# Kernel optimization log

Hardware: AMD Instinct MI355X
Metric: run time of the kernel (lower is better)

The kernel has to match this reference:

```python
import jax, jax.numpy as jnp
import numpy as np

DIM = 768
H = 12
HD = DIM // H
SCALE = HD ** (-0.5)


def setup_inputs() -> dict:
    key = jax.random.key(0)
    ks = jax.random.split(key, 10)
    s = DIM ** (-0.5)
    x = jax.random.normal(ks[0], (8, 1024, DIM), dtype=jnp.float32)
    Wq = jax.random.normal(ks[1], (DIM, DIM), dtype=jnp.float32) * s
    Wk = jax.random.normal(ks[2], (DIM, DIM), dtype=jnp.float32) * s
    Wv = jax.random.normal(ks[3], (DIM, DIM), dtype=jnp.float32) * s
    Wl = jax.random.normal(ks[4], (H, H), dtype=jnp.float32) * (H ** -0.5)
    bl = jax.random.normal(ks[5], (H,), dtype=jnp.float32) * 0.02
    Ww = jax.random.normal(ks[6], (H, H), dtype=jnp.float32) * (H ** -0.5)
    bw = jax.random.normal(ks[7], (H,), dtype=jnp.float32) * 0.02
    Wp = jax.random.normal(ks[8], (DIM, DIM), dtype=jnp.float32) * s
    bp = jax.random.normal(ks[9], (DIM,), dtype=jnp.float32) * 0.02
    return {"x": x, "Wq": Wq, "Wk": Wk, "Wv": Wv, "Wl": Wl, "bl": bl,
            "Ww": Ww, "bw": bw, "Wp": Wp, "bp": bp}


def reference(x, Wq, Wk, Wv, Wl, bl, Ww, bw, Wp, bp):
    B, N, C = x.shape
    # QKV projections (no bias), split heads -> (B, H, N, hd)
    q = (x @ Wq).reshape(B, N, H, HD).transpose(0, 2, 1, 3) * SCALE
    k = (x @ Wk).reshape(B, N, H, HD).transpose(0, 2, 1, 3)
    v = (x @ Wv).reshape(B, N, H, HD).transpose(0, 2, 1, 3)
    # scores: (B, H, N, N)
    attn = jnp.einsum('bhid,bhjd->bhij', q, k)
    # talking heads pre-softmax: mix over head axis (Linear on last dim of BNNH)
    attn = jnp.einsum('bhij,gh->bgij', attn, Wl) + bl[None, :, None, None]
    attn = jax.nn.softmax(attn, axis=-1)
    # talking heads post-softmax
    attn = jnp.einsum('bhij,gh->bgij', attn, Ww) + bw[None, :, None, None]
    out = jnp.einsum('bhij,bhjd->bhid', attn, v)  # (B, H, N, hd)
    out = out.transpose(0, 2, 1, 3).reshape(B, N, C)
    return out @ Wp + bp
```

## Files before the change

kernel.cpp:

```cpp
#include <hip/hip_runtime.h>
#include <hip/hip_bf16.h>

#define DIM 768
#define NH 12
#define HD 64
#define SEQ 1024
#define BATCH 8
#define LOG2E 1.44269504f

typedef __bf16 bf16x8 __attribute__((ext_vector_type(8)));
typedef _Float16 f16x4 __attribute__((ext_vector_type(4)));
typedef float f32x4 __attribute__((ext_vector_type(4)));

__device__ __forceinline__ void gload_lds16(const __bf16* g, __bf16* l) {
  __builtin_amdgcn_global_load_lds(
      (const __attribute__((address_space(1))) void*)g,
      (__attribute__((address_space(3))) void*)l, 16, 0, 0);
}

__global__ __launch_bounds__(256) void xcvt(
    const float* __restrict__ X, __bf16* __restrict__ Xb)
{
  const size_t i = ((size_t)blockIdx.x * 256 + threadIdx.x) * 8;
  float4 a0 = *(const float4*)(X + i);
  float4 a1 = *(const float4*)(X + i + 4);
  bf16x8 v = { (__bf16)a0.x, (__bf16)a0.y, (__bf16)a0.z, (__bf16)a0.w,
               (__bf16)a1.x, (__bf16)a1.y, (__bf16)a1.z, (__bf16)a1.w };
  *(bf16x8*)(Xb + i) = v;
}

__global__ __launch_bounds__(256) void wtrans(
    const float* __restrict__ Wq, const float* __restrict__ Wk,
    const float* __restrict__ Wv, const float* __restrict__ Wp,
    __bf16* __restrict__ Tq, __bf16* __restrict__ Tk,
    __bf16* __restrict__ Tv, __bf16* __restrict__ Tp)
{
  const int z = blockIdx.z;
  const float* W = (z==0) ? Wq : (z==1) ? Wk : (z==2) ? Wv : Wp;
  __bf16* T = (z==0) ? Tq : (z==1) ? Tk : (z==2) ? Tv : Tp;
  __shared__ float tile[32][33];
  const int t = threadIdx.x, tx = t & 31, ty = t >> 5;
  const int k0 = blockIdx.y * 32, n0 = blockIdx.x * 32;
#pragma unroll
  for (int u = 0; u < 4; ++u)
    tile[ty + u*8][tx] = W[(size_t)(k0 + ty + u*8) * DIM + n0 + tx];
  __syncthreads();
#pragma unroll
  for (int u = 0; u < 4; ++u)
    T[(size_t)(n0 + ty + u*8) * DIM + k0 + tx] = (__bf16)tile[tx][ty + u*8];
}

__global__ __launch_bounds__(256) void gemm_qkv(
    const __bf16* __restrict__ Xb, const __bf16* __restrict__ WT,
    __bf16* __restrict__ Qo, __bf16* __restrict__ Ko, _Float16* __restrict__ Vt2)
{
  __shared__ __bf16 As[128 * 32];
  __shared__ __bf16 Bs[128 * 32];

  const int t = threadIdx.x, lane = t & 63, w = t >> 6;
  const int n16 = lane & 15, q = lane >> 4;
  const int m0 = blockIdx.y * 128, n0 = blockIdx.x * 128;
  const int wm = (w >> 1) * 64, wn = (w & 1) * 64;

  const int srow = t >> 2, scol = (t & 3) * 8;
  const __bf16* Ag = Xb + (size_t)(m0 + srow) * DIM + scol;
  const __bf16* Bg = WT + (size_t)(n0 + srow) * DIM + scol;
  __bf16* AsW0 = &As[w * 512];
  __bf16* AsW1 = &As[2048 + w * 512];
  __bf16* BsW0 = &Bs[w * 512];
  __bf16* BsW1 = &Bs[2048 + w * 512];

  f32x4 acc[4][4];
#pragma unroll
  for (int mt = 0; mt < 4; ++mt)
#pragma unroll
    for (int nt = 0; nt < 4; ++nt) acc[mt][nt] = (f32x4){0.f,0.f,0.f,0.f};

  for (int kb = 0; kb < DIM; kb += 32) {
    __syncthreads();
    gload_lds16(Ag + kb, AsW0);
    gload_lds16(Ag + (size_t)64 * DIM + kb, AsW1);
    gload_lds16(Bg + kb, BsW0);
    gload_lds16(Bg + (size_t)64 * DIM + kb, BsW1);
    __syncthreads();

    bf16x8 af[4], bg[4];
#pragma unroll
    for (int mt = 0; mt < 4; ++mt)
      af[mt] = *(const bf16x8*)&As[(wm + mt*16 + n16) * 32 + q*8];
#pragma unroll
    for (int nt = 0; nt < 4; ++nt)
      bg[nt] = *(const bf16x8*)&Bs[(wn + nt*16 + n16) * 32 + q*8];
#pragma unroll
    for (int mt = 0; mt < 4; ++mt)
#pragma unroll
      for (int nt = 0; nt < 4; ++nt)
        acc[mt][nt] = __builtin_amdgcn_mfma_f32_16x16x32_bf16(af[mt], bg[nt], acc[mt][nt], 0, 0, 0);
  }

#pragma unroll
  for (int nt = 0; nt < 4; ++nt) {
    const int n = n0 + wn + nt*16 + n16;
    const int z = n / DIM, c = n % DIM;
    const int h = c >> 6, d = c & 63;
#pragma unroll
    for (int mt = 0; mt < 4; ++mt) {
#pragma unroll
      for (int r = 0; r < 4; ++r) {
        const int row = m0 + wm + mt*16 + q*4 + r;
        const int bb = row >> 10, ii = row & 1023;
        const float v = acc[mt][nt][r];
        if (z == 0)
          Qo[(((size_t)bb*NH + h)*SEQ + ii)*HD + d] = (__bf16)(v * 0.125f);
        else if (z == 1)
          Ko[(((size_t)bb*NH + h)*SEQ + ii)*HD + d] = (__bf16)v;
        else
          Vt2[((((size_t)bb*NH + h)*64 + (ii >> 4))*HD + d)*16 + (ii & 15)] = (_Float16)v;
      }
    }
  }
}

__global__ __launch_bounds__(256, 2) void attn_fused(
    const __bf16* __restrict__ Qg, const __bf16* __restrict__ Kg,
    const _Float16* __restrict__ Vt2,
    const float* __restrict__ Wl, const float* __restrict__ bl,
    const float* __restrict__ Ww, const float* __restrict__ bw,
    __bf16* __restrict__ Aout)
{
  __shared__ _Float16 Sl[2][12][324];
  __shared__ _Float16 Pl[2][16 * 248];

  const int t = threadIdx.x, lane = t & 63, w = t >> 6;
  const int n16 = lane & 15, q = lane >> 4;
  const int h0 = w * 3;
  const int b = blockIdx.x, i0 = blockIdx.y * 16;
  const size_t bbase = (size_t)b * NH * SEQ * HD;

  f16x4 wlA, wwA;
  f32x4 blC, bwC;
#pragma unroll
  for (int j = 0; j < 4; ++j) {
    const int k = q*4 + j;
    wlA[j] = (n16 < 12 && k < 12) ? (_Float16)(Wl[n16*12 + k] * LOG2E) : (_Float16)0.f;
    wwA[j] = (n16 < 12 && k < 12) ? (_Float16)Ww[n16*12 + k] : (_Float16)0.f;
    blC[j] = (k < 12) ? bl[k] * LOG2E : 0.f;
    bwC[j] = (k < 12) ? bw[k] : 0.f;
  }

  bf16x8 qf[3][2];
#pragma unroll
  for (int hh = 0; hh < 3; ++hh)
#pragma unroll
    for (int cc = 0; cc < 2; ++cc)
      qf[hh][cc] = *(const bf16x8*)(Qg + bbase + ((size_t)(h0+hh)*SEQ + i0 + n16)*HD + cc*32 + q*8);

  const f32x4 z4 = {0.f, 0.f, 0.f, 0.f};

  float lrun[4][4];
#pragma unroll
  for (int c = 0; c < 4; ++c)
#pragma unroll
    for (int r = 0; r < 4; ++r) lrun[c][r] = 0.f;

  bf16x8 kC[3][2], kN[3][2];
#pragma unroll
  for (int hh = 0; hh < 3; ++hh) {
    const __bf16* kp = Kg + bbase + ((size_t)(h0+hh)*SEQ + n16)*HD + q*8;
    kC[hh][0] = *(const bf16x8*)kp;
    kC[hh][1] = *(const bf16x8*)(kp + 32);
  }

#pragma unroll 2
  for (int jt = 0; jt < SEQ/16; ++jt) {
    const int buf = jt & 1;
    const int jn = (jt < SEQ/16 - 1) ? jt + 1 : jt;
#pragma unroll
    for (int hh = 0; hh < 3; ++hh) {
      const __bf16* kp = Kg + bbase + ((size_t)(h0+hh)*SEQ + jn*16 + n16)*HD + q*8;
      kN[hh][0] = *(const bf16x8*)kp;
      kN[hh][1] = *(const bf16x8*)(kp + 32);
    }
    __builtin_amdgcn_s_setprio(1);
#pragma unroll
    for (int hh = 0; hh < 3; ++hh) {
      f32x4 s = __builtin_amdgcn_mfma_f32_16x16x32_bf16(kC[hh][0], qf[hh][0], z4, 0, 0, 0);
      s = __builtin_amdgcn_mfma_f32_16x16x32_bf16(kC[hh][1], qf[hh][1], s, 0, 0, 0);
      f16x4 sh = { (_Float16)s[0], (_Float16)s[1], (_Float16)s[2], (_Float16)s[3] };
      *(f16x4*)&Sl[buf][h0+hh][n16*20 + q*4] = sh;
    }
    __builtin_amdgcn_s_setprio(0);
    __syncthreads();
#pragma unroll
    for (int c = 0; c < 4; ++c) {
      const int i = w*4 + c;
      f16x4 sf;
#pragma unroll
      for (int dd = 0; dd < 4; ++dd) {
        int h = q*4 + dd; if (h > 11) h = 11;
        sf[dd] = Sl[buf][h][i*20 + n16];
      }
      f32x4 sm = __builtin_amdgcn_mfma_f32_16x16x16f16(wlA, sf, blC, 0, 0, 0);
#pragma unroll
      for (int r = 0; r < 4; ++r) lrun[c][r] += __builtin_amdgcn_exp2f(sm[r]);
    }
#pragma unroll
    for (int hh = 0; hh < 3; ++hh) { kC[hh][0] = kN[hh][0]; kC[hh][1] = kN[hh][1]; }
  }

  float linv[4][4];
#pragma unroll
  for (int c = 0; c < 4; ++c)
#pragma unroll
    for (int r = 0; r < 4; ++r) {
      float l = lrun[c][r];
      l += __shfl_xor(l, 1);
      l += __shfl_xor(l, 2);
      l += __shfl_xor(l, 4);
      l += __shfl_xor(l, 8);
      linv[c][r] = 1.0f / l;
    }

  f32x4 oacc[3][4];
#pragma unroll
  for (int hh = 0; hh < 3; ++hh)
#pragma unroll
    for (int dc = 0; dc < 4; ++dc) oacc[hh][dc] = z4;

  f16x4 vC[3][4], vN[3][4];
#pragma unroll
  for (int hh = 0; hh < 3; ++hh) {
    const __bf16* kp = Kg + bbase + ((size_t)(h0+hh)*SEQ + n16)*HD + q*8;
    kC[hh][0] = *(const bf16x8*)kp;
    kC[hh][1] = *(const bf16x8*)(kp + 32);
  }

#pragma unroll 2
  for (int jt = 0; jt < SEQ/16; ++jt) {
    const int buf = jt & 1;
    const int jn = (jt < SEQ/16 - 1) ? jt + 1 : jt;
#pragma unroll
    for (int hh = 0; hh < 3; ++hh) {
      const __bf16* kp = Kg + bbase + ((size_t)(h0+hh)*SEQ + jn*16 + n16)*HD + q*8;
      kN[hh][0] = *(const bf16x8*)kp;
      kN[hh][1] = *(const bf16x8*)(kp + 32);
    }
#pragma unroll
    for (int hh = 0; hh < 3; ++hh) {
      const _Float16* vb = Vt2 + (((size_t)(b*NH + h0 + hh)*64 + jt)*HD)*16;
#pragma unroll
      for (int dc = 0; dc < 4; ++dc)
        vN[hh][dc] = *(const f16x4*)(vb + (size_t)(dc*16 + n16)*16 + q*4);
    }
    __builtin_amdgcn_s_setprio(1);
#pragma unroll
    for (int hh = 0; hh < 3; ++hh) {
      f32x4 s = __builtin_amdgcn_mfma_f32_16x16x32_bf16(kC[hh][0], qf[hh][0], z4, 0, 0, 0);
      s = __builtin_amdgcn_mfma_f32_16x16x32_bf16(kC[hh][1], qf[hh][1], s, 0, 0, 0);
      f16x4 sh = { (_Float16)s[0], (_Float16)s[1], (_Float16)s[2], (_Float16)s[3] };
      *(f16x4*)&Sl[buf][h0+hh][n16*20 + q*4] = sh;
    }
    __builtin_amdgcn_s_setprio(0);
    __syncthreads();
    if (jt > 0) {
      f16x4 pa[3];
#pragma unroll
      for (int hh = 0; hh < 3; ++hh)
        pa[hh] = *(const f16x4*)&Pl[1 - buf][n16*248 + (h0+hh)*20 + q*4];
      __builtin_amdgcn_s_setprio(1);
#pragma unroll
      for (int hh = 0; hh < 3; ++hh)
#pragma unroll
        for (int dc = 0; dc < 4; ++dc)
          oacc[hh][dc] = __builtin_amdgcn_mfma_f32_16x16x16f16(pa[hh], vC[hh][dc], oacc[hh][dc], 0, 0, 0);
      __builtin_amdgcn_s_setprio(0);
    }
#pragma unroll
    for (int c = 0; c < 4; ++c) {
      const int i = w*4 + c;
      f16x4 sf;
#pragma unroll
      for (int dd = 0; dd < 4; ++dd) {
        int h = q*4 + dd; if (h > 11) h = 11;
        sf[dd] = Sl[buf][h][i*20 + n16];
      }
      f32x4 sm = __builtin_amdgcn_mfma_f32_16x16x16f16(wlA, sf, blC, 0, 0, 0);
      f16x4 pnf;
#pragma unroll
      for (int r = 0; r < 4; ++r)
        pnf[r] = (_Float16)(__builtin_amdgcn_exp2f(sm[r]) * linv[c][r]);
      f32x4 p2 = __builtin_amdgcn_mfma_f32_16x16x16f16(wwA, pnf, bwC, 0, 0, 0);
      if (q < 3) {
#pragma unroll
        for (int r = 0; r < 4; ++r)
          Pl[buf][i*248 + (q*4 + r)*20 + n16] = (_Float16)p2[r];
      }
    }
#pragma unroll
    for (int hh = 0; hh < 3; ++hh) {
      kC[hh][0] = kN[hh][0]; kC[hh][1] = kN[hh][1];
#pragma unroll
      for (int dc = 0; dc < 4; ++dc) vC[hh][dc] = vN[hh][dc];
    }
  }
  __syncthreads();
#pragma unroll
  for (int hh = 0; hh < 3; ++hh) {
    const int g2 = h0 + hh;
    f16x4 pa = *(const f16x4*)&Pl[1][n16*248 + g2*20 + q*4];
#pragma unroll
    for (int dc = 0; dc < 4; ++dc)
      oacc[hh][dc] = __builtin_amdgcn_mfma_f32_16x16x16f16(pa, vC[hh][dc], oacc[hh][dc], 0, 0, 0);
  }

#pragma unroll
  for (int hh = 0; hh < 3; ++hh)
#pragma unroll
    for (int dc = 0; dc < 4; ++dc)
#pragma unroll
      for (int r = 0; r < 4; ++r)
        Aout[((size_t)(b*SEQ + i0 + q*4 + r))*DIM + (h0+hh)*HD + dc*16 + n16] =
            (__bf16)oacc[hh][dc][r];
}

__global__ __launch_bounds__(256) void gemm_proj(
    const __bf16* __restrict__ A, const __bf16* __restrict__ WpT,
    const float* __restrict__ bp, float* __restrict__ Out)
{
  __shared__ __bf16 As[128 * 32];
  __shared__ __bf16 Bs[128 * 32];

  const int t = threadIdx.x, lane = t & 63, w = t >> 6;
  const int n16 = lane & 15, q = lane >> 4;
  const int m0 = blockIdx.y * 128, n0 = blockIdx.x * 128;
  const int wm = (w >> 1) * 64, wn = (w & 1) * 64;

  const int srow = t >> 2, scol = (t & 3) * 8;
  const __bf16* Ag = A + (size_t)(m0 + srow) * DIM + scol;
  const __bf16* Bg = WpT + (size_t)(n0 + srow) * DIM + scol;
  __bf16* AsW0 = &As[w * 512];
  __bf16* AsW1 = &As[2048 + w * 512];
  __bf16* BsW0 = &Bs[w * 512];
  __bf16* BsW1 = &Bs[2048 + w * 512];

  f32x4 acc[4][4];
#pragma unroll
  for (int nt = 0; nt < 4; ++nt) {
    const float bpv = bp[n0 + wn + nt*16 + n16];
#pragma unroll
    for (int mt = 0; mt < 4; ++mt)
#pragma unroll
      for (int r = 0; r < 4; ++r) acc[mt][nt][r] = bpv;
  }

  for (int kb = 0; kb < DIM; kb += 32) {
    __syncthreads();
    gload_lds16(Ag + kb, AsW0);
    gload_lds16(Ag + (size_t)64 * DIM + kb, AsW1);
    gload_lds16(Bg + kb, BsW0);
    gload_lds16(Bg + (size_t)64 * DIM + kb, BsW1);
    __syncthreads();

    bf16x8 af[4], bg[4];
#pragma unroll
    for (int mt = 0; mt < 4; ++mt)
      af[mt] = *(const bf16x8*)&As[(wm + mt*16 + n16) * 32 + q*8];
#pragma unroll
    for (int nt = 0; nt < 4; ++nt)
      bg[nt] = *(const bf16x8*)&Bs[(wn + nt*16 + n16) * 32 + q*8];
#pragma unroll
    for (int mt = 0; mt < 4; ++mt)
#pragma unroll
      for (int nt = 0; nt < 4; ++nt)
        acc[mt][nt] = __builtin_amdgcn_mfma_f32_16x16x32_bf16(af[mt], bg[nt], acc[mt][nt], 0, 0, 0);
  }

#pragma unroll
  for (int nt = 0; nt < 4; ++nt) {
    const int n = n0 + wn + nt*16 + n16;
#pragma unroll
    for (int mt = 0; mt < 4; ++mt)
#pragma unroll
      for (int r = 0; r < 4; ++r) {
        const int row = m0 + wm + mt*16 + q*4 + r;
        Out[(size_t)row * DIM + n] = acc[mt][nt][r];
      }
  }
}

extern "C" void kernel_launch(void* const* d_in, const int* in_sizes, int n_in,
                              void* d_out, int out_size, void* d_ws, size_t ws_size,
                              hipStream_t stream) {
  const float* x  = (const float*)d_in[0];
  const float* Wq = (const float*)d_in[1];
  const float* Wk = (const float*)d_in[2];
  const float* Wv = (const float*)d_in[3];
  const float* Wl = (const float*)d_in[4];
  const float* bl = (const float*)d_in[5];
  const float* Ww = (const float*)d_in[6];
  const float* bw = (const float*)d_in[7];
  const float* Wp = (const float*)d_in[8];
  const float* bp = (const float*)d_in[9];

  char* p = (char*)d_ws;
  const size_t WSZ = (size_t)DIM * DIM * 2;
  const size_t TSZ = (size_t)BATCH * NH * SEQ * HD * 2;
  __bf16*   WqT = (__bf16*)p;            p += WSZ;
  __bf16*   WkT = (__bf16*)p;            p += WSZ;
  __bf16*   WvT = (__bf16*)p;            p += WSZ;
  __bf16*   WpT = (__bf16*)p;            p += WSZ;
  __bf16*   Q   = (__bf16*)p;            p += TSZ;
  __bf16*   K   = (__bf16*)p;            p += TSZ;
  _Float16* V2  = (_Float16*)p;          p += TSZ;
  __bf16*   AO  = (__bf16*)p;            p += TSZ;
  __bf16*   Xb  = (__bf16*)p;            p += TSZ;

  xcvt<<<dim3((BATCH*SEQ*DIM)/(256*8)), 256, 0, stream>>>(x, Xb);
  wtrans<<<dim3(24, 24, 4), 256, 0, stream>>>(Wq, Wk, Wv, Wp, WqT, WkT, WvT, WpT);
  gemm_qkv<<<dim3(18, 64), 256, 0, stream>>>(Xb, WqT, Q, K, V2);
  attn_fused<<<dim3(BATCH, SEQ/16), 256, 0, stream>>>(Q, K, V2, Wl, bl, Ww, bw, AO);
  gemm_proj<<<dim3(6, 64), 256, 0, stream>>>(AO, WpT, bp, (float*)d_out);
}
```

Measured before the change: 422.9 us.

## Compute softmax row sums with per-wave key splits, removing first-pass barriers

The first pass that accumulates softmax denominators is restructured. Each wave now handles all 12 heads for a quarter of the key tiles, mixes heads in fp32 registers using Wl kept in LDS, and accumulates exp2 sums without any per-tile __syncthreads. Partial sums are combined across waves once through a small LDS buffer. This removes 64 block barriers and the LDS round-trip from the first pass, at the cost of 24 Q fragments held in registers plus scalar FMAs in place of a head-mixing MFMA, which may raise register pressure.

```diff
diff --git a/kernel.cpp b/kernel.cpp
--- a/kernel.cpp
+++ b/kernel.cpp
@@ -130,12 +130,18 @@
 {
   __shared__ _Float16 Sl[2][12][324];
   __shared__ _Float16 Pl[2][16 * 248];
+  __shared__ float Wls[144];
+  __shared__ float blS[12];
+  __shared__ float Lx[4][12][16];
 
   const int t = threadIdx.x, lane = t & 63, w = t >> 6;
   const int n16 = lane & 15, q = lane >> 4;
   const int h0 = w * 3;
   const int b = blockIdx.x, i0 = blockIdx.y * 16;
   const size_t bbase = (size_t)b * NH * SEQ * HD;
+
+  if (t < 144) Wls[t] = Wl[t] * LOG2E;
+  if (t < 12)  blS[t] = bl[t] * LOG2E;
 
   f16x4 wlA, wwA;
   f32x4 blC, bwC;
@@ -148,6 +154,83 @@
     bwC[j] = (k < 12) ? bw[k] : 0.f;
   }
 
+  const f32x4 z4 = {0.f, 0.f, 0.f, 0.f};
+  __syncthreads();
+
+  bf16x8 qA0[12], qA1[12];
+#pragma unroll
+  for (int h = 0; h < 12; ++h) {
+    const __bf16* qp = Qg + bbase + ((size_t)h*SEQ + i0 + n16)*HD + q*8;
+    qA0[h] = *(const bf16x8*)qp;
+    qA1[h] = *(const bf16x8*)(qp + 32);
+  }
+
+  float lsum[12];
+#pragma unroll
+  for (int g = 0; g < 12; ++g) lsum[g] = 0.f;
+
+  for (int tt = 0; tt < 16; ++tt) {
+    const int jt = tt*4 + w;
+    f32x4 sh[12];
+#pragma unroll
+    for (int h = 0; h < 12; ++h) {
+      const __bf16* kp = Kg + bbase + ((size_t)h*SEQ + jt*16 + n16)*HD + q*8;
+      bf16x8 k0 = *(const bf16x8*)kp;
+      bf16x8 k1 = *(const bf16x8*)(kp + 32);
+      f32x4 s = __builtin_amdgcn_mfma_f32_16x16x32_bf16(k0, qA0[h], z4, 0, 0, 0);
+      sh[h] = __builtin_amdgcn_mfma_f32_16x16x32_bf16(k1, qA1[h], s, 0, 0, 0);
+    }
+#pragma unroll
+    for (int g = 0; g < 12; ++g) {
+      const f32x4 wr0 = *(const f32x4*)&Wls[g*12];
+      const f32x4 wr1 = *(const f32x4*)&Wls[g*12 + 4];
+      const f32x4 wr2 = *(const f32x4*)&Wls[g*12 + 8];
+      f32x4 a = { blS[g], blS[g], blS[g], blS[g] };
+#pragma unroll
+      for (int h = 0; h < 4; ++h)
+#pragma unroll
+        for (int r = 0; r < 4; ++r) a[r] += wr0[h] * sh[h][r];
+#pragma unroll
+      for (int h = 0; h < 4; ++h)
+#pragma unroll
+        for (int r = 0; r < 4; ++r) a[r] += wr1[h] * sh[4+h][r];
+#pragma unroll
+      for (int h = 0; h < 4; ++h)
+#pragma unroll
+        for (int r = 0; r < 4; ++r) a[r] += wr2[h] * sh[8+h][r];
+      lsum[g] += __builtin_amdgcn_exp2f(a[0]) + __builtin_amdgcn_exp2f(a[1])
+               + __builtin_amdgcn_exp2f(a[2]) + __builtin_amdgcn_exp2f(a[3]);
+    }
+  }
+
+#pragma unroll
+  for (int g = 0; g < 12; ++g) {
+    float l = lsum[g];
+    l += __shfl_xor(l, 16);
+    l += __shfl_xor(l, 32);
+    lsum[g] = l;
+  }
+  if (lane < 16) {
+#pragma unroll
+    for (int g = 0; g < 12; ++g) Lx[w][g][lane] = lsum[g];
+  }
+  __syncthreads();
+
+  float linv[4][4];
+#pragma unroll
+  for (int c = 0; c < 4; ++c)
+#pragma unroll
+    for (int r = 0; r < 4; ++r) {
+      const int g = q*4 + r;
+      if (g < 12) {
+        const int i = w*4 + c;
+        float l = Lx[0][g][i] + Lx[1][g][i] + Lx[2][g][i] + Lx[3][g][i];
+        linv[c][r] = 1.0f / l;
+      } else {
+        linv[c][r] = 0.f;
+      }
+    }
+
   bf16x8 qf[3][2];
 #pragma unroll
   for (int hh = 0; hh < 3; ++hh)
@@ -155,15 +238,14 @@
     for (int cc = 0; cc < 2; ++cc)
       qf[hh][cc] = *(const bf16x8*)(Qg + bbase + ((size_t)(h0+hh)*SEQ + i0 + n16)*HD + cc*32 + q*8);
 
-  const f32x4 z4 = {0.f, 0.f, 0.f, 0.f};
-
-  float lrun[4][4];
-#pragma unroll
-  for (int c = 0; c < 4; ++c)
-#pragma unroll
-    for (int r = 0; r < 4; ++r) lrun[c][r] = 0.f;
+  f32x4 oacc[3][4];
+#pragma unroll
+  for (int hh = 0; hh < 3; ++hh)
+#pragma unroll
+    for (int dc = 0; dc < 4; ++dc) oacc[hh][dc] = z4;
 
   bf16x8 kC[3][2], kN[3][2];
+  f16x4 vC[3][4], vN[3][4];
 #pragma unroll
   for (int hh = 0; hh < 3; ++hh) {
     const __bf16* kp = Kg + bbase + ((size_t)(h0+hh)*SEQ + n16)*HD + q*8;
@@ -181,84 +263,20 @@
       kN[hh][0] = *(const bf16x8*)kp;
       kN[hh][1] = *(const bf16x8*)(kp + 32);
     }
+#pragma unroll
+    for (int hh = 0; hh < 3; ++hh) {
+      const _Float16* vb = Vt2 + (((size_t)(b*NH + h0 + hh)*64 + jt)*HD)*16;
+#pragma unroll
+      for (int dc = 0; dc < 4; ++dc)
+        vN[hh][dc] = *(const f16x4*)(vb + (size_t)(dc*16 + n16)*16 + q*4);
+    }
     __builtin_amdgcn_s_setprio(1);
 #pragma unroll
     for (int hh = 0; hh < 3; ++hh) {
       f32x4 s = __builtin_amdgcn_mfma_f32_16x16x32_bf16(kC[hh][0], qf[hh][0], z4, 0, 0, 0);
       s = __builtin_amdgcn_mfma_f32_16x16x32_bf16(kC[hh][1], qf[hh][1], s, 0, 0, 0);
-      f16x4 sh = { (_Float16)s[0], (_Float16)s[1], (_Float16)s[2], (_Float16)s[3] };
-      *(f16x4*)&Sl[buf][h0+hh][n16*20 + q*4] = sh;
-    }
-    __builtin_amdgcn_s_setprio(0);
-    __syncthreads();
-#pragma unroll
-    for (int c = 0; c < 4; ++c) {
-      const int i = w*4 + c;
-      f16x4 sf;
-#pragma unroll
-      for (int dd = 0; dd < 4; ++dd) {
-        int h = q*4 + dd; if (h > 11) h = 11;
-        sf[dd] = Sl[buf][h][i*20 + n16];
-      }
-      f32x4 sm = __builtin_amdgcn_mfma_f32_16x16x16f16(wlA, sf, blC, 0, 0, 0);
-#pragma unroll
-      for (int r = 0; r < 4; ++r) lrun[c][r] += __builtin_amdgcn_exp2f(sm[r]);
-    }
-#pragma unroll
-    for (int hh = 0; hh < 3; ++hh) { kC[hh][0] = kN[hh][0]; kC[hh][1] = kN[hh][1]; }
-  }
-
-  float linv[4][4];
-#pragma unroll
-  for (int c = 0; c < 4; ++c)
-#pragma unroll
-    for (int r = 0; r < 4; ++r) {
-      float l = lrun[c][r];
-      l += __shfl_xor(l, 1);
-      l += __shfl_xor(l, 2);
-      l += __shfl_xor(l, 4);
-      l += __shfl_xor(l, 8);
-      linv[c][r] = 1.0f / l;
-    }
-
-  f32x4 oacc[3][4];
-#pragma unroll
-  for (int hh = 0; hh < 3; ++hh)
-#pragma unroll
-    for (int dc = 0; dc < 4; ++dc) oacc[hh][dc] = z4;
-
-  f16x4 vC[3][4], vN[3][4];
-#pragma unroll
-  for (int hh = 0; hh < 3; ++hh) {
-    const __bf16* kp = Kg + bbase + ((size_t)(h0+hh)*SEQ + n16)*HD + q*8;
-    kC[hh][0] = *(const bf16x8*)kp;
-    kC[hh][1] = *(const bf16x8*)(kp + 32);
-  }
-
-#pragma unroll 2
-  for (int jt = 0; jt < SEQ/16; ++jt) {
-    const int buf = jt & 1;
-    const int jn = (jt < SEQ/16 - 1) ? jt + 1 : jt;
-#pragma unroll
-    for (int hh = 0; hh < 3; ++hh) {
-      const __bf16* kp = Kg + bbase + ((size_t)(h0+hh)*SEQ + jn*16 + n16)*HD + q*8;
-      kN[hh][0] = *(const bf16x8*)kp;
-      kN[hh][1] = *(const bf16x8*)(kp + 32);
-    }
-#pragma unroll
-    for (int hh = 0; hh < 3; ++hh) {
-      const _Float16* vb = Vt2 + (((size_t)(b*NH + h0 + hh)*64 + jt)*HD)*16;
-#pragma unroll
-      for (int dc = 0; dc < 4; ++dc)
-        vN[hh][dc] = *(const f16x4*)(vb + (size_t)(dc*16 + n16)*16 + q*4);
-    }
-    __builtin_amdgcn_s_setprio(1);
-#pragma unroll
-    for (int hh = 0; hh < 3; ++hh) {
-      f32x4 s = __builtin_amdgcn_mfma_f32_16x16x32_bf16(kC[hh][0], qf[hh][0], z4, 0, 0, 0);
-      s = __builtin_amdgcn_mfma_f32_16x16x32_bf16(kC[hh][1], qf[hh][1], s, 0, 0, 0);
-      f16x4 sh = { (_Float16)s[0], (_Float16)s[1], (_Float16)s[2], (_Float16)s[3] };
-      *(f16x4*)&Sl[buf][h0+hh][n16*20 + q*4] = sh;
+      f16x4 sh2 = { (_Float16)s[0], (_Float16)s[1], (_Float16)s[2], (_Float16)s[3] };
+      *(f16x4*)&Sl[buf][h0+hh][n16*20 + q*4] = sh2;
     }
     __builtin_amdgcn_s_setprio(0);
     __syncthreads();
```

After: 524.4 us. 1.24x slower.
